# Optimization experiments

Measured on AMD Instinct MI355X. Metric: run time of the kernel, lower is better.

Reference implementation:

```python
import jax, jax.numpy as jnp
import numpy as np

BN_EPS = 1e-5

def batchnorm(x, gamma, beta):
    # training-mode BN over axis 0 with biased variance (matches torch)
    mean = jnp.mean(x, axis=0)
    var = jnp.var(x, axis=0)
    return (x - mean) * jax.lax.rsqrt(var + BN_EPS) * gamma + beta

def setup_inputs() -> dict:
    key = jax.random.key(0)
    ks = jax.random.split(key, 8)
    N, M, A, B = 50000, 12, 64, 41
    atom_in_fea = jax.random.normal(ks[0], (N, A), dtype=jnp.float32)
    nbr_fea = jax.random.normal(ks[1], (N, M, B), dtype=jnp.float32)
    nbr_fea_idx = jax.random.randint(ks[2], (N, M), 0, N)
    fan_in = 2 * A + B
    lim = 1.0 / np.sqrt(fan_in)
    W = jax.random.uniform(ks[3], (2 * A, fan_in), minval=-lim, maxval=lim, dtype=jnp.float32)
    b = jax.random.uniform(ks[4], (2 * A,), minval=-lim, maxval=lim, dtype=jnp.float32)
    bn1_g = jnp.ones((2 * A,), jnp.float32)
    bn1_b = jnp.zeros((2 * A,), jnp.float32)
    bn2_g = jnp.ones((A,), jnp.float32)
    bn2_b = jnp.zeros((A,), jnp.float32)
    return {"atom_in_fea": atom_in_fea, "nbr_fea": nbr_fea, "nbr_fea_idx": nbr_fea_idx,
            "W": W, "b": b, "bn1_g": bn1_g, "bn1_b": bn1_b, "bn2_g": bn2_g, "bn2_b": bn2_b}

def reference(atom_in_fea, nbr_fea, nbr_fea_idx, W, b, bn1_g, bn1_b, bn2_g, bn2_b):
    N, M = nbr_fea_idx.shape
    A = atom_in_fea.shape[1]
    atom_nbr_fea = atom_in_fea[nbr_fea_idx]                       # (N, M, A) gather
    self_fea = jnp.broadcast_to(atom_in_fea[:, None, :], (N, M, A))
    total_nbr_fea = jnp.concatenate([self_fea, atom_nbr_fea, nbr_fea], axis=2)  # (N,M,2A+B)
    total_gated = jnp.einsum('nmf,of->nmo', total_nbr_fea, W) + b  # (N,M,2A)
    total_gated = batchnorm(total_gated.reshape(-1, 2 * A), bn1_g, bn1_b).reshape(N, M, 2 * A)
    nbr_filter, nbr_core = total_gated[..., :A], total_gated[..., A:]
    nbr_sumed = jnp.sum(jax.nn.sigmoid(nbr_filter) * jax.nn.softplus(nbr_core), axis=1)  # (N,A)
    nbr_sumed = batchnorm(nbr_sumed, bn2_g, bn2_b)
    return jax.nn.softplus(atom_in_fea + nbr_sumed)
```

## Files before the change

kernel.cpp:

```cpp
#include <hip/hip_runtime.h>
#include <math.h>

#define N_ATOMS 50000
#define M_NBR   12
#define A_FEA   64
#define B_FEA   41
#define KF      169
#define KP      192
#define LDA     200
#define OC      128
#define NROW    600000
#define TR32    32
#define NT32    18750
#define NT192   3125
#define BN_EPS  1e-5f
#define L2E     1.44269504088896340736f
#define LN2     0.693147180559945309417f

#define WS_SUM1   0
#define WS_SUMSQ1 128
#define WS_SUM2   256
#define WS_SUMSQ2 320
#define WS_NFLOAT 384
#define WS_GATED_OFF 2048ull
#define GATED_BYTES  ((size_t)NT32 * 512 * 16)

#define BAR_LGKM() asm volatile("s_waitcnt lgkmcnt(0)\n\ts_barrier" ::: "memory")

typedef __attribute__((ext_vector_type(8))) short s16x8;
typedef __attribute__((ext_vector_type(4))) float f32x4;

__device__ __forceinline__ float fsigmoid(float x) {
    float e = __builtin_amdgcn_exp2f(-x * L2E);
    return __builtin_amdgcn_rcpf(1.f + e);
}
__device__ __forceinline__ float fsoftplus(float x) {
    float e = __builtin_amdgcn_exp2f(-fabsf(x) * L2E);
    return fmaxf(x, 0.f) + __builtin_amdgcn_logf(1.f + e) * LN2;
}
__device__ __forceinline__ unsigned int pack2bf(float lo, float hi) {
    unsigned int r;
    asm("v_cvt_pk_bf16_f32 %0, %1, %2" : "=v"(r) : "v"(lo), "v"(hi));
    return r;
}
__device__ __forceinline__ unsigned short f2bf(float f) {
    unsigned int r;
    asm("v_cvt_pk_bf16_f32 %0, %1, %1" : "=v"(r) : "v"(f));
    return (unsigned short)r;
}
__device__ __forceinline__ float bf_lo(unsigned int u) { return __uint_as_float(u << 16); }
__device__ __forceinline__ float bf_hi(unsigned int u) { return __uint_as_float(u & 0xFFFF0000u); }

__global__ void k_zero(float* __restrict__ dout, float* __restrict__ stats) {
    int i = blockIdx.x * blockDim.x + threadIdx.x;
    int stride = gridDim.x * blockDim.x;
    for (int j = i; j < N_ATOMS * A_FEA; j += stride) dout[j] = 0.f;
    if (i < WS_NFLOAT) stats[i] = 0.f;
}

struct TileRegs {
    float4 selfv[2];
    float4 gat[2];
    float4 bond0, bond1;
};

__device__ __forceinline__ void issue_selfbond(TileRegs& R, const float* __restrict__ atom,
                                               const float* __restrict__ nbr,
                                               int rb, int r16, int k4, int tid) {
#pragma unroll
    for (int it = 0; it < 2; ++it) {
        int row = rb + r16 + it * 16;
        R.selfv[it] = *(const float4*)(atom + ((unsigned)row / 12u) * A_FEA + k4);
    }
    const float* bb = nbr + (size_t)rb * B_FEA;
    R.bond0 = *(const float4*)(bb + (size_t)tid * 4);
    if (tid < 72) R.bond1 = *(const float4*)(bb + (size_t)(256 + tid) * 4);
}
__device__ __forceinline__ void issue_gat(TileRegs& R, const float* __restrict__ atom,
                                          const int nbi[2], int k4) {
#pragma unroll
    for (int it = 0; it < 2; ++it)
        R.gat[it] = *(const float4*)(atom + (unsigned)nbi[it] * A_FEA + k4);
}
__device__ __forceinline__ void write_tile(unsigned short* __restrict__ At,
                                           const TileRegs& R, int r16, int k4, int tid) {
#pragma unroll
    for (int it = 0; it < 2; ++it) {
        int r = r16 + it * 16;
        uint2 u;
        u.x = pack2bf(R.selfv[it].x, R.selfv[it].y);
        u.y = pack2bf(R.selfv[it].z, R.selfv[it].w);
        *(uint2*)&At[r * LDA + k4] = u;
        uint2 v;
        v.x = pack2bf(R.gat[it].x, R.gat[it].y);
        v.y = pack2bf(R.gat[it].z, R.gat[it].w);
        *(uint2*)&At[r * LDA + A_FEA + k4] = v;
    }
    {
        const float bv[4] = {R.bond0.x, R.bond0.y, R.bond0.z, R.bond0.w};
#pragma unroll
        for (int e = 0; e < 4; ++e) {
            int le = tid * 4 + e;
            unsigned r = (unsigned)le / 41u, j = (unsigned)le - r * 41u;
            At[r * LDA + 2 * A_FEA + j] = f2bf(bv[e]);
        }
    }
    if (tid < 72) {
        const float bv[4] = {R.bond1.x, R.bond1.y, R.bond1.z, R.bond1.w};
#pragma unroll
        for (int e = 0; e < 4; ++e) {
            int le = 1024 + tid * 4 + e;
            unsigned r = (unsigned)le / 41u, j = (unsigned)le - r * 41u;
            At[r * LDA + 2 * A_FEA + j] = f2bf(bv[e]);
        }
    }
}

template <bool STORE>
__global__ __launch_bounds__(256, 3)
void k_gemm_spill(const float* __restrict__ atom, const float* __restrict__ nbr,
                  const int* __restrict__ idx, const float* __restrict__ W,
                  float* __restrict__ stats, uint4* __restrict__ gated) {
    __shared__ __align__(16) unsigned short At[2][TR32 * LDA];
    const int tid = threadIdx.x;
    for (int i = tid; i < 2 * TR32 * (KP - KF); i += 256) {
        int b  = i / (TR32 * (KP - KF));
        int ii = i - b * (TR32 * (KP - KF));
        int r  = ii / (KP - KF);
        int j  = KF + ii - r * (KP - KF);
        At[b][r * LDA + j] = 0;
    }
    const int lane = tid & 63, gg = tid >> 6;
    const int col  = lane & 15, q8 = (lane >> 4) * 8;
    const int r16  = tid >> 4;
    const int k4   = (tid & 15) * 4;

    s16x8 bfr[2][6];
#pragma unroll
    for (int tt = 0; tt < 2; ++tt) {
        const float* wr = W + ((gg + tt * 4) * 16 + col) * KF;
#pragma unroll
        for (int kc = 0; kc < 6; ++kc) {
            int kb = kc * 32 + q8;
            s16x8 f;
#pragma unroll
            for (int j = 0; j < 8; ++j) {
                int k = kb + j;
                f[j] = (short)f2bf(k < KF ? wr[k] : 0.f);
            }
            bfr[tt][kc] = f;
        }
    }

    const int base = NT32 / gridDim.x;
    const int rem  = NT32 % gridDim.x;
    const int bid  = blockIdx.x;
    const int tA   = bid * base + min(bid, rem);
    const int tB   = tA + base + (bid < rem ? 1 : 0);

    float s[2] = {0.f, 0.f}, q[2] = {0.f, 0.f};
    TileRegs R;
    int nbiN[2];
    if (tA < tB) {
        int rb = tA * TR32;
        int nbiC[2] = {idx[rb + r16], idx[rb + r16 + 16]};
        issue_selfbond(R, atom, nbr, rb, r16, k4, tid);
        issue_gat(R, atom, nbiC, k4);
        if (tA + 1 < tB) {
            int rb1 = rb + TR32;
            nbiN[0] = idx[rb1 + r16]; nbiN[1] = idx[rb1 + r16 + 16];
        }
    }
    int p = 0;
    for (int t = tA; t < tB; ++t) {
        write_tile(At[p], R, r16, k4, tid);
        if (t + 1 < tB) {
            issue_selfbond(R, atom, nbr, (t + 1) * TR32, r16, k4, tid);
            issue_gat(R, atom, nbiN, k4);
            if (t + 2 < tB) {
                int rb2 = (t + 2) * TR32;
                nbiN[0] = idx[rb2 + r16]; nbiN[1] = idx[rb2 + r16 + 16];
            }
        }
        BAR_LGKM();
        const unsigned short* A = At[p];
        f32x4 acc[2][2];
#pragma unroll
        for (int rt = 0; rt < 2; ++rt)
#pragma unroll
            for (int tt = 0; tt < 2; ++tt) acc[rt][tt] = (f32x4){0.f, 0.f, 0.f, 0.f};
#pragma unroll
        for (int kc = 0; kc < 6; ++kc) {
            const int k0 = kc * 32;
            const s16x8 a0 = *(const s16x8*)&A[(col) * LDA + k0 + q8];
            const s16x8 a1 = *(const s16x8*)&A[(16 + col) * LDA + k0 + q8];
#pragma unroll
            for (int tt = 0; tt < 2; ++tt) {
                acc[0][tt] = __builtin_amdgcn_mfma_f32_16x16x32_bf16(a0, bfr[tt][kc], acc[0][tt], 0, 0, 0);
                acc[1][tt] = __builtin_amdgcn_mfma_f32_16x16x32_bf16(a1, bfr[tt][kc], acc[1][tt], 0, 0, 0);
            }
        }
#pragma unroll
        for (int tt = 0; tt < 2; ++tt)
#pragma unroll
            for (int rt = 0; rt < 2; ++rt)
#pragma unroll
                for (int e = 0; e < 4; ++e) {
                    float v = acc[rt][tt][e];
                    s[tt] += v; q[tt] = fmaf(v, v, q[tt]);
                }
        if (STORE) {
#pragma unroll
            for (int rt = 0; rt < 2; ++rt) {
                uint4 u;
                u.x = pack2bf(acc[rt][0][0], acc[rt][0][1]);
                u.y = pack2bf(acc[rt][0][2], acc[rt][0][3]);
                u.z = pack2bf(acc[rt][1][0], acc[rt][1][1]);
                u.w = pack2bf(acc[rt][1][2], acc[rt][1][3]);
                gated[(size_t)t * 512 + rt * 256 + tid] = u;
            }
        }
        p ^= 1;
    }
#pragma unroll
    for (int tt = 0; tt < 2; ++tt) {
        float sv = s[tt], qv = q[tt];
        sv += __shfl_xor(sv, 16); sv += __shfl_xor(sv, 32);
        qv += __shfl_xor(qv, 16); qv += __shfl_xor(qv, 32);
        if (lane < 16) {
            int c = (gg + tt * 4) * 16 + col;
            atomicAdd(&stats[WS_SUM1 + c], sv);
            atomicAdd(&stats[WS_SUMSQ1 + c], qv);
        }
    }
}

__global__ __launch_bounds__(256, 3)
void k_apply(const uint4* __restrict__ gated,
             const float* __restrict__ g1, const float* __restrict__ b1,
             float* __restrict__ stats, float* __restrict__ dout) {
    __shared__ float red[512];
    const int tid = threadIdx.x;
    const int c   = tid & 63;
    const int w   = tid >> 6;
    const int col = c & 15, gg = c >> 4;

    const float invn = 1.f / (float)NROW;
    float meanF = stats[WS_SUM1 + c] * invn;
    float varF  = stats[WS_SUMSQ1 + c] * invn - meanF * meanF;
    float scF   = g1[c] * rsqrtf(varF + BN_EPS), shF = b1[c] - meanF * scF;
    const int cc = c + 64;
    float meanC = stats[WS_SUM1 + cc] * invn;
    float varC  = stats[WS_SUMSQ1 + cc] * invn - meanC * meanC;
    float scC   = g1[cc] * rsqrtf(varC + BN_EPS), shC = b1[cc] - meanC * scC;

    float bs = 0.f, bq = 0.f;
    for (int T = blockIdx.x; T < NT192; T += gridDim.x) {
        uint4 G[4][3];
#pragma unroll
        for (int j = 0; j < 4; ++j) {
            const int a = j * 4 + w;
#pragma unroll
            for (int l = 0; l < 3; ++l) {
                const int Gi  = 3 * a + l;
                const int sub = Gi >> 3, rt = (Gi >> 2) & 1, q = Gi & 3;
                G[j][l] = gated[(size_t)(T * 6 + sub) * 512 + rt * 256
                                + gg * 64 + q * 16 + col];
            }
        }
#pragma unroll
        for (int j = 0; j < 4; ++j) {
            float sum = 0.f;
#pragma unroll
            for (int l = 0; l < 3; ++l) {
                const uint4 u = G[j][l];
                const float fv[4] = {bf_lo(u.x), bf_hi(u.x), bf_lo(u.y), bf_hi(u.y)};
                const float cv[4] = {bf_lo(u.z), bf_hi(u.z), bf_lo(u.w), bf_hi(u.w)};
#pragma unroll
                for (int e = 0; e < 4; ++e) {
                    float gF = fmaf(fv[e], scF, shF);
                    float gC = fmaf(cv[e], scC, shC);
                    sum += fsigmoid(gF) * fsoftplus(gC);
                }
            }
            const int a = j * 4 + w;
            dout[((size_t)T * 16 + a) * 64 + c] = sum;
            bs += sum; bq = fmaf(sum, sum, bq);
        }
    }
    red[tid] = bs; red[256 + tid] = bq;
    __syncthreads();
    if (tid < 64) {
        float ss = red[tid] + red[tid + 64] + red[tid + 128] + red[tid + 192];
        float qq = red[256 + tid] + red[256 + tid + 64] + red[256 + tid + 128] + red[256 + tid + 192];
        atomicAdd(&stats[WS_SUM2 + tid], ss);
        atomicAdd(&stats[WS_SUMSQ2 + tid], qq);
    }
}

__global__ __launch_bounds__(256, 2)
void k_gemm_main(const float* __restrict__ atom, const float* __restrict__ nbr,
                 const int* __restrict__ idx, const float* __restrict__ W,
                 const float* __restrict__ g1, const float* __restrict__ b1,
                 const float* __restrict__ stats, float* __restrict__ dout) {
    __shared__ __align__(16) unsigned short At[TR32 * LDA];
    __shared__ float S[4 * 64];
    const int tid = threadIdx.x;
    for (int i = tid; i < TR32 * (KP - KF); i += 256) {
        int r = i / (KP - KF), j = KF + i - r * (KP - KF);
        At[r * LDA + j] = 0;
    }
    for (int i = tid; i < 4 * 64; i += 256) S[i] = 0.f;
    const int lane = tid & 63, gg = tid >> 6;
    const int col = lane & 15, q8 = (lane >> 4) * 8, quad = lane >> 4;
    const int r16 = tid >> 4, k4 = (tid & 15) * 4;

    s16x8 bfr[2][6];
#pragma unroll
    for (int tt = 0; tt < 2; ++tt) {
        const float* wr = W + ((gg + tt * 4) * 16 + col) * KF;
#pragma unroll
        for (int kc = 0; kc < 6; ++kc) {
            int kb = kc * 32 + q8;
            s16x8 f;
#pragma unroll
            for (int j = 0; j < 8; ++j) { int k = kb + j; f[j] = (short)f2bf(k < KF ? wr[k] : 0.f); }
            bfr[tt][kc] = f;
        }
    }
    const float invn = 1.f / (float)NROW;
    float sc[2], sh[2];
#pragma unroll
    for (int tt = 0; tt < 2; ++tt) {
        int c = (gg + tt * 4) * 16 + col;
        float mean = stats[WS_SUM1 + c] * invn;
        float var  = stats[WS_SUMSQ1 + c] * invn - mean * mean;
        sc[tt] = g1[c] * rsqrtf(var + BN_EPS);
        sh[tt] = b1[c] - mean * sc[tt];
    }
    const int per = (NT32 + gridDim.x - 1) / gridDim.x;
    const int tA = blockIdx.x * per, tB = min(NT32, tA + per);
    for (int t = tA; t < tB; ++t) {
        const int rb = t * TR32;
        __syncthreads();
        {
            TileRegs R;
            int nbiC[2] = {idx[rb + r16], idx[rb + r16 + 16]};
            issue_selfbond(R, atom, nbr, rb, r16, k4, tid);
            issue_gat(R, atom, nbiC, k4);
            write_tile(At, R, r16, k4, tid);
        }
        __syncthreads();
        f32x4 acc[2][2];
#pragma unroll
        for (int rt = 0; rt < 2; ++rt)
#pragma unroll
            for (int tt = 0; tt < 2; ++tt) acc[rt][tt] = (f32x4){0.f, 0.f, 0.f, 0.f};
#pragma unroll
        for (int kc = 0; kc < 6; ++kc) {
            const int k0 = kc * 32;
            const s16x8 a0 = *(const s16x8*)&At[(col) * LDA + k0 + q8];
            const s16x8 a1 = *(const s16x8*)&At[(16 + col) * LDA + k0 + q8];
#pragma unroll
            for (int tt = 0; tt < 2; ++tt) {
                acc[0][tt] = __builtin_amdgcn_mfma_f32_16x16x32_bf16(a0, bfr[tt][kc], acc[0][tt], 0, 0, 0);
                acc[1][tt] = __builtin_amdgcn_mfma_f32_16x16x32_bf16(a1, bfr[tt][kc], acc[1][tt], 0, 0, 0);
            }
        }
        const int a0i = rb / M_NBR;
#pragma unroll
        for (int rt = 0; rt < 2; ++rt)
#pragma unroll
            for (int e = 0; e < 4; ++e) {
                float gF = fmaf(acc[rt][0][e], sc[0], sh[0]);
                float gC = fmaf(acc[rt][1][e], sc[1], sh[1]);
                float v  = fsigmoid(gF) * fsoftplus(gC);
                int row = rb + rt * 16 + quad * 4 + e;
                atomicAdd(&S[(row / M_NBR - a0i) * 64 + gg * 16 + col], v);
            }
        __syncthreads();
        const int amax = (rb + TR32 - 1) / M_NBR - a0i;
        for (int i = tid; i < 4 * 64; i += 256) {
            float v = S[i];
            S[i] = 0.f;
            int a = i >> 6;
            if (a <= amax) atomicAdd(&dout[(a0i + a) * 64 + (i & 63)], v);
        }
    }
}

__global__ __launch_bounds__(256, 1)
void k_bn2_stats(const float* __restrict__ dout, float* __restrict__ stats) {
    int tid = threadIdx.x;
    int c = tid & 63;
    int g = tid >> 6;
    float s = 0.f, q = 0.f;
    for (int n = blockIdx.x * 4 + g; n < N_ATOMS; n += gridDim.x * 4) {
        float v = dout[n * 64 + c];
        s += v; q = fmaf(v, v, q);
    }
    __shared__ float red[4][64];
    red[g][c] = s;
    __syncthreads();
    if (g == 0)
        atomicAdd(&stats[WS_SUM2 + c], red[0][c] + red[1][c] + red[2][c] + red[3][c]);
    __syncthreads();
    red[g][c] = q;
    __syncthreads();
    if (g == 0)
        atomicAdd(&stats[WS_SUMSQ2 + c], red[0][c] + red[1][c] + red[2][c] + red[3][c]);
}

__global__ void k_final(const float* __restrict__ atom, const float* __restrict__ g2,
                        const float* __restrict__ b2, const float* __restrict__ stats,
                        float* __restrict__ dout) {
    int i0 = blockIdx.x * blockDim.x + threadIdx.x;
    int c = i0 & 63;
    const float invn = 1.f / (float)N_ATOMS;
    float mean = stats[WS_SUM2 + c] * invn;
    float var  = stats[WS_SUMSQ2 + c] * invn - mean * mean;
    float sc   = g2[c] * rsqrtf(var + BN_EPS);
    float sh   = b2[c] - mean * sc;
    int stride = gridDim.x * blockDim.x;
    for (int i = i0; i < N_ATOMS * A_FEA; i += stride) {
        float v = fmaf(dout[i], sc, sh) + atom[i];
        dout[i] = fsoftplus(v);
    }
}

extern "C" void kernel_launch(void* const* d_in, const int* in_sizes, int n_in,
                              void* d_out, int out_size, void* d_ws, size_t ws_size,
                              hipStream_t stream) {
    const float* atom = (const float*)d_in[0];
    const float* nbr  = (const float*)d_in[1];
    const int*   idx  = (const int*)d_in[2];
    const float* W    = (const float*)d_in[3];
    const float* g1   = (const float*)d_in[5];
    const float* b1   = (const float*)d_in[6];
    const float* g2   = (const float*)d_in[7];
    const float* b2   = (const float*)d_in[8];
    float* dout  = (float*)d_out;
    float* stats = (float*)d_ws;
    uint4* gated = (uint4*)((char*)d_ws + WS_GATED_OFF);

    const bool fused = ws_size >= (WS_GATED_OFF + GATED_BYTES);

    if (fused) {
        hipMemsetAsync(stats, 0, WS_NFLOAT * sizeof(float), stream);
        k_gemm_spill<true><<<750, 256, 0, stream>>>(atom, nbr, idx, W, stats, gated);
        k_apply<<<625, 256, 0, stream>>>(gated, g1, b1, stats, dout);
        k_final<<<512, 256, 0, stream>>>(atom, g2, b2, stats, dout);
    } else {
        k_zero<<<512, 256, 0, stream>>>(dout, stats);
        k_gemm_spill<false><<<750, 256, 0, stream>>>(atom, nbr, idx, W, stats, nullptr);
        k_gemm_main<<<1024, 256, 0, stream>>>(atom, nbr, idx, W, g1, b1, stats, dout);
        k_bn2_stats<<<256, 256, 0, stream>>>(dout, stats);
        k_final<<<512, 256, 0, stream>>>(atom, g2, b2, stats, dout);
    }
}
```

Baseline: 260.0 us.

## Precompute per-atom self and neighbor projections, shrink edge GEMM to bond features

The linear layer is split algebraically. A new kernel computes per-atom projections of the self and neighbor halves of W once per atom (N rows instead of N*M). The edge kernel then runs a GEMM only over the 41 bond features and adds a gathered precomputed neighbor projection plus the self projection. This removes about two thirds of the per-edge MFMA work and the gather of 64-wide atom features. In exchange it adds an extra kernel and workspace traffic for the float2 projection tables, and it only runs when the workspace is large enough for them.

Result: slower. 297.9 us (+14.6%).

```diff
diff --git a/kernel.cpp b/kernel.cpp
--- a/kernel.cpp
+++ b/kernel.cpp
@@ -8,11 +8,15 @@
 #define KF      169
 #define KP      192
 #define LDA     200
+#define KB3     41
+#define KPB     64
+#define LDB     72
 #define OC      128
 #define NROW    600000
 #define TR32    32
 #define NT32    18750
 #define NT192   3125
+#define NPT     3125
 #define BN_EPS  1e-5f
 #define L2E     1.44269504088896340736f
 #define LN2     0.693147180559945309417f
@@ -24,6 +28,10 @@
 #define WS_NFLOAT 384
 #define WS_GATED_OFF 2048ull
 #define GATED_BYTES  ((size_t)NT32 * 512 * 16)
+#define WS_PSELF_OFF (WS_GATED_OFF + GATED_BYTES)
+#define PSELF_BYTES  ((size_t)N_ATOMS * 64 * 8)
+#define WS_PGAT_OFF  (WS_PSELF_OFF + PSELF_BYTES)
+#define PGAT_BYTES   PSELF_BYTES
 
 #define BAR_LGKM() asm volatile("s_waitcnt lgkmcnt(0)\n\ts_barrier" ::: "memory")
 
@@ -58,12 +66,224 @@
     if (i < WS_NFLOAT) stats[i] = 0.f;
 }
 
+__global__ __launch_bounds__(256, 3)
+void k_p12(const float* __restrict__ atom, const float* __restrict__ W,
+           float2* __restrict__ Pself, float2* __restrict__ Pgat) {
+    __shared__ __align__(16) unsigned short At[16 * LDB];
+    const int tid = threadIdx.x;
+    const int lane = tid & 63, w = tid >> 6;
+    const int col = lane & 15, quad = lane >> 4, q8 = quad * 8;
+    const int r = tid >> 4, k4 = (tid & 15) * 4;
+
+    s16x8 frag[4][2];
+#pragma unroll
+    for (int tt = 0; tt < 4; ++tt) {
+        const int o = (w + tt * 4) * 16 + col;
+        const float* wr = (o < 128) ? (W + (size_t)o * KF)
+                                    : (W + (size_t)(o - 128) * KF + 64);
+#pragma unroll
+        for (int kc = 0; kc < 2; ++kc) {
+            const int kb = kc * 32 + q8;
+            s16x8 f;
+#pragma unroll
+            for (int j = 0; j < 8; ++j) f[j] = (short)f2bf(wr[kb + j]);
+            frag[tt][kc] = f;
+        }
+    }
+    for (int T = blockIdx.x; T < NPT; T += gridDim.x) {
+        const int ab = T * 16;
+        float4 v = *(const float4*)(atom + (size_t)(ab + r) * A_FEA + k4);
+        __syncthreads();
+        uint2 u;
+        u.x = pack2bf(v.x, v.y);
+        u.y = pack2bf(v.z, v.w);
+        *(uint2*)&At[r * LDB + k4] = u;
+        BAR_LGKM();
+        f32x4 acc[4];
+#pragma unroll
+        for (int tt = 0; tt < 4; ++tt) acc[tt] = (f32x4){0.f, 0.f, 0.f, 0.f};
+#pragma unroll
+        for (int kc = 0; kc < 2; ++kc) {
+            const s16x8 a = *(const s16x8*)&At[col * LDB + kc * 32 + q8];
+#pragma unroll
+            for (int tt = 0; tt < 4; ++tt)
+                acc[tt] = __builtin_amdgcn_mfma_f32_16x16x32_bf16(a, frag[tt][kc], acc[tt], 0, 0, 0);
+        }
+#pragma unroll
+        for (int e = 0; e < 4; ++e) {
+            const int a_ = ab + quad * 4 + e;
+            const int c  = w * 16 + col;
+            Pself[(size_t)a_ * 64 + c] = make_float2(acc[0][e], acc[1][e]);
+            Pgat [(size_t)a_ * 64 + c] = make_float2(acc[2][e], acc[3][e]);
+        }
+    }
+}
+
+template <bool STORE>
+__global__ __launch_bounds__(256, 3)
+void k_bgemm(const float* __restrict__ nbr, const int* __restrict__ idx,
+             const float* __restrict__ W,
+             const float2* __restrict__ Pself, const float2* __restrict__ Pgat,
+             float* __restrict__ stats, uint4* __restrict__ gated) {
+    __shared__ __align__(16) unsigned short At[2][TR32 * LDB];
+    const int tid = threadIdx.x;
+    for (int i = tid; i < 2 * TR32 * (KPB - KB3); i += 256) {
+        int b  = i / (TR32 * (KPB - KB3));
+        int ii = i - b * (TR32 * (KPB - KB3));
+        int r  = ii / (KPB - KB3);
+        int j  = KB3 + ii - r * (KPB - KB3);
+        At[b][r * LDB + j] = 0;
+    }
+    const int lane = tid & 63, gg = tid >> 6;
+    const int col  = lane & 15, quad = lane >> 4, q8 = quad * 8;
+    const int c0   = gg * 16 + col;
+
+    s16x8 bfr[2][2];
+#pragma unroll
+    for (int tt = 0; tt < 2; ++tt) {
+        const float* wr = W + (size_t)((gg + tt * 4) * 16 + col) * KF + 128;
+#pragma unroll
+        for (int kc = 0; kc < 2; ++kc) {
+            const int kb = kc * 32 + q8;
+            s16x8 f;
+#pragma unroll
+            for (int j = 0; j < 8; ++j)
+                f[j] = (short)((kb + j < KB3) ? f2bf(wr[kb + j]) : (unsigned short)0);
+            bfr[tt][kc] = f;
+        }
+    }
+    const int base = NT32 / gridDim.x, rem = NT32 % gridDim.x, bid = blockIdx.x;
+    const int tA = bid * base + min(bid, rem);
+    const int tB = tA + base + (bid < rem ? 1 : 0);
+
+    float s0 = 0.f, q0 = 0.f, s1 = 0.f, q1 = 0.f;
+    float4 bond0, bond1;
+    int idxC[8], idxN[8];
+    if (tA < tB) {
+        const float* bb = nbr + (size_t)tA * TR32 * KB3;
+        bond0 = *(const float4*)(bb + (size_t)tid * 4);
+        if (tid < 72) bond1 = *(const float4*)(bb + (size_t)(256 + tid) * 4);
+#pragma unroll
+        for (int rt = 0; rt < 2; ++rt) {
+            int4 ii = *(const int4*)&idx[tA * TR32 + rt * 16 + quad * 4];
+            idxC[rt * 4 + 0] = ii.x; idxC[rt * 4 + 1] = ii.y;
+            idxC[rt * 4 + 2] = ii.z; idxC[rt * 4 + 3] = ii.w;
+        }
+        if (tA + 1 < tB) {
+#pragma unroll
+            for (int rt = 0; rt < 2; ++rt) {
+                int4 ii = *(const int4*)&idx[(tA + 1) * TR32 + rt * 16 + quad * 4];
+                idxN[rt * 4 + 0] = ii.x; idxN[rt * 4 + 1] = ii.y;
+                idxN[rt * 4 + 2] = ii.z; idxN[rt * 4 + 3] = ii.w;
+            }
+        }
+    }
+    int p = 0;
+    for (int t = tA; t < tB; ++t) {
+        const int rb = t * TR32;
+        float2 pg[8];
+#pragma unroll
+        for (int sl = 0; sl < 8; ++sl)
+            pg[sl] = Pgat[(size_t)idxC[sl] * 64 + c0];
+#pragma unroll
+        for (int sl = 0; sl < 8; ++sl) idxC[sl] = idxN[sl];
+        if (t + 2 < tB) {
+#pragma unroll
+            for (int rt = 0; rt < 2; ++rt) {
+                int4 ii = *(const int4*)&idx[(t + 2) * TR32 + rt * 16 + quad * 4];
+                idxN[rt * 4 + 0] = ii.x; idxN[rt * 4 + 1] = ii.y;
+                idxN[rt * 4 + 2] = ii.z; idxN[rt * 4 + 3] = ii.w;
+            }
+        }
+        {
+            const float bv0[4] = {bond0.x, bond0.y, bond0.z, bond0.w};
+#pragma unroll
+            for (int e = 0; e < 4; ++e) {
+                int le = tid * 4 + e;
+                unsigned r = (unsigned)le / 41u, j = (unsigned)le - r * 41u;
+                At[p][r * LDB + j] = f2bf(bv0[e]);
+            }
+            if (tid < 72) {
+                const float bv1[4] = {bond1.x, bond1.y, bond1.z, bond1.w};
+#pragma unroll
+                for (int e = 0; e < 4; ++e) {
+                    int le = 1024 + tid * 4 + e;
+                    unsigned r = (unsigned)le / 41u, j = (unsigned)le - r * 41u;
+                    At[p][r * LDB + j] = f2bf(bv1[e]);
+                }
+            }
+        }
+        if (t + 1 < tB) {
+            const float* bb = nbr + (size_t)(t + 1) * TR32 * KB3;
+            bond0 = *(const float4*)(bb + (size_t)tid * 4);
+            if (tid < 72) bond1 = *(const float4*)(bb + (size_t)(256 + tid) * 4);
+        }
+        BAR_LGKM();
+        const unsigned short* A = At[p];
+        f32x4 acc[2][2];
+#pragma unroll
+        for (int rt = 0; rt < 2; ++rt)
+#pragma unroll
+            for (int tt = 0; tt < 2; ++tt) acc[rt][tt] = (f32x4){0.f, 0.f, 0.f, 0.f};
+#pragma unroll
+        for (int kc = 0; kc < 2; ++kc) {
+            const int k0 = kc * 32;
+            const s16x8 a0 = *(const s16x8*)&A[(col) * LDB + k0 + q8];
+            const s16x8 a1 = *(const s16x8*)&A[(16 + col) * LDB + k0 + q8];
+#pragma unroll
+            for (int tt = 0; tt < 2; ++tt) {
+                acc[0][tt] = __builtin_amdgcn_mfma_f32_16x16x32_bf16(a0, bfr[tt][kc], acc[0][tt], 0, 0, 0);
+                acc[1][tt] = __builtin_amdgcn_mfma_f32_16x16x32_bf16(a1, bfr[tt][kc], acc[1][tt], 0, 0, 0);
+            }
+        }
+#pragma unroll
+        for (int rt = 0; rt < 2; ++rt) {
+            float F[4], C[4];
+#pragma unroll
+            for (int e = 0; e < 4; ++e) {
+                const int r = rt * 16 + quad * 4 + e;
+                const unsigned n = (unsigned)(rb + r) / 12u;
+                const float2 ps  = Pself[(size_t)n * 64 + c0];
+                const float2 pgv = pg[rt * 4 + e];
+                F[e] = acc[rt][0][e] + ps.x + pgv.x;
+                C[e] = acc[rt][1][e] + ps.y + pgv.y;
+                s0 += F[e]; q0 = fmaf(F[e], F[e], q0);
+                s1 += C[e]; q1 = fmaf(C[e], C[e], q1);
+            }
+            if (STORE) {
+                uint4 u;
+                u.x = pack2bf(F[0], F[1]);
+                u.y = pack2bf(F[2], F[3]);
+                u.z = pack2bf(C[0], C[1]);
+                u.w = pack2bf(C[2], C[3]);
+                gated[(size_t)t * 512 + rt * 256 + tid] = u;
+            }
+        }
+        p ^= 1;
+    }
+    {
+        float sv = s0, qv = q0;
+        sv += __shfl_xor(sv, 16); sv += __shfl_xor(sv, 32);
+        qv += __shfl_xor(qv, 16); qv += __shfl_xor(qv, 32);
+        if (lane < 16) {
+            atomicAdd(&stats[WS_SUM1 + c0], sv);
+            atomicAdd(&stats[WS_SUMSQ1 + c0], qv);
+        }
+        sv = s1; qv = q1;
+        sv += __shfl_xor(sv, 16); sv += __shfl_xor(sv, 32);
+        qv += __shfl_xor(qv, 16); qv += __shfl_xor(qv, 32);
+        if (lane < 16) {
+            atomicAdd(&stats[WS_SUM1 + c0 + 64], sv);
+            atomicAdd(&stats[WS_SUMSQ1 + c0 + 64], qv);
+        }
+    }
+}
+
 struct TileRegs {
     float4 selfv[2];
     float4 gat[2];
     float4 bond0, bond1;
 };
-
 __device__ __forceinline__ void issue_selfbond(TileRegs& R, const float* __restrict__ atom,
                                                const float* __restrict__ nbr,
                                                int rb, int r16, int k4, int tid) {
@@ -151,12 +371,9 @@
             bfr[tt][kc] = f;
         }
     }
-
-    const int base = NT32 / gridDim.x;
-    const int rem  = NT32 % gridDim.x;
-    const int bid  = blockIdx.x;
-    const int tA   = bid * base + min(bid, rem);
-    const int tB   = tA + base + (bid < rem ? 1 : 0);
+    const int base = NT32 / gridDim.x, rem = NT32 % gridDim.x, bid = blockIdx.x;
+    const int tA = bid * base + min(bid, rem);
+    const int tB = tA + base + (bid < rem ? 1 : 0);
 
     float s[2] = {0.f, 0.f}, q[2] = {0.f, 0.f};
     TileRegs R;
@@ -442,10 +659,19 @@
     float* dout  = (float*)d_out;
     float* stats = (float*)d_ws;
     uint4* gated = (uint4*)((char*)d_ws + WS_GATED_OFF);
-
-    const bool fused = ws_size >= (WS_GATED_OFF + GATED_BYTES);
-
-    if (fused) {
+    float2* Pself = (float2*)((char*)d_ws + WS_PSELF_OFF);
+    float2* Pgat  = (float2*)((char*)d_ws + WS_PGAT_OFF);
+
+    const bool decomposed = ws_size >= (WS_PGAT_OFF + PGAT_BYTES);
+    const bool fused      = ws_size >= (WS_GATED_OFF + GATED_BYTES);
+
+    if (decomposed) {
+        hipMemsetAsync(stats, 0, WS_NFLOAT * sizeof(float), stream);
+        k_p12<<<625, 256, 0, stream>>>(atom, W, Pself, Pgat);
+        k_bgemm<true><<<750, 256, 0, stream>>>(nbr, idx, W, Pself, Pgat, stats, gated);
+        k_apply<<<625, 256, 0, stream>>>(gated, g1, b1, stats, dout);
+        k_final<<<512, 256, 0, stream>>>(atom, g2, b2, stats, dout);
+    } else if (fused) {
         hipMemsetAsync(stats, 0, WS_NFLOAT * sizeof(float), stream);
         k_gemm_spill<true><<<750, 256, 0, stream>>>(atom, nbr, idx, W, stats, gated);
         k_apply<<<625, 256, 0, stream>>>(gated, g1, b1, stats, dout);
```
